# Kernel tuning notes

Hardware: AMD Instinct MI355X
Metric: run time of the kernel (lower is better)

The kernel has to match this reference:

```python
import jax, jax.numpy as jnp
import numpy as np

N = 100000   # nodes
H = 128      # hidden_size
T = 32       # transitivity_size
MD = 16      # mask_dim
K = 3        # propagation steps
E_S = 600000 # spatial edges
E_D = 600000 # dom edges


def setup_inputs() -> dict:
    key = jax.random.key(0)
    ks = jax.random.split(key, 12)
    return {
        "x": jax.random.normal(ks[0], (N, H), jnp.float32),
        "mask": jax.random.uniform(ks[1], (N, MD), jnp.float32),
        "spatial_edge_index": jax.random.randint(ks[2], (2, E_S), 0, N, jnp.int64 if jax.config.jax_enable_x64 else jnp.int32),
        "dom_edge_index": jax.random.randint(ks[3], (2, E_D), 0, N, jnp.int64 if jax.config.jax_enable_x64 else jnp.int32),
        "spatial_edge_attr": jax.random.normal(ks[4], (E_S, 4), jnp.float32),
        "dom_edge_attr": jax.random.normal(ks[5], (E_D, 1), jnp.float32),
        "W_trans": jax.random.normal(ks[6], (2 * H, T), jnp.float32) / np.sqrt(2 * H),
        "b_trans": jnp.zeros((T,), jnp.float32),
        "W_pos": jax.random.normal(ks[7], (4 + T, 1), jnp.float32) / np.sqrt(4 + T),
        "b_pos": jnp.zeros((1,), jnp.float32),
        "W_dom": jax.random.normal(ks[8], (1 + T, 1), jnp.float32) / np.sqrt(1 + T),
        "b_dom": jnp.zeros((1,), jnp.float32),
    }


def _edge_attrs(x, edge_index, W, b):
    # EdgeAttrs: gather src/dst node features, concat, linear + tanh -> [E, T]
    h = jnp.concatenate([x[edge_index[0]], x[edge_index[1]]], axis=1)
    return jnp.tanh(h @ W + b)


def _edge_mask(edge_attr, mask, edge_index, W, b, k_steps, n_nodes):
    # EdgeMask: per-edge gating weight in (0,1), then K rounds of
    # gate-weighted max-propagation of the node mask along edges.
    ew = jax.nn.sigmoid(edge_attr @ W + b)  # [E, 1]
    src, dst = edge_index[0], edge_index[1]
    m = mask
    for _ in range(k_steps):
        msg = m[src] * ew                                  # [E, MD]
        agg = jax.ops.segment_max(msg, dst, num_segments=n_nodes)
        m = jnp.maximum(m, agg)                            # -inf (empty segs) absorbed
    return m, ew


def reference(x, mask, spatial_edge_index, dom_edge_index, spatial_edge_attr,
              dom_edge_attr, W_trans, b_trans, W_pos, b_pos, W_dom, b_dom):
    n_nodes = x.shape[0]
    # spatial branch (projection is dom -> no safe_bc_edges broadcast)
    trans_s = _edge_attrs(x, spatial_edge_index, W_trans, b_trans)
    pos_in = jnp.concatenate([spatial_edge_attr, trans_s], axis=1)  # [E_S, 4+T]
    pos_mask, _pos_ew = _edge_mask(pos_in, mask, spatial_edge_index, W_pos, b_pos, K, n_nodes)
    # dom branch
    trans_d = _edge_attrs(x, dom_edge_index, W_trans, b_trans)
    dom_in = jnp.concatenate([dom_edge_attr, trans_d], axis=1)      # [E_D, 1+T]
    dom_mask, _dom_ew = _edge_mask(dom_in, mask, dom_edge_index, W_dom, b_dom, K, n_nodes)
    return jnp.maximum(mask, jnp.maximum(pos_mask, dom_mask))
```

## Files before the change

kernel.cpp:

```cpp
#include <hip/hip_runtime.h>
#include <hip/hip_bf16.h>
#include <stdint.h>

#define NNODES 100000
#define HID 128
#define TSZ 32
#define MDIM 16
#define ES 600000
#define ED 600000
#define ETOT (ES + ED)
#define GN (2 * NNODES)
#define GNP 200704
#define SCAN_BLOCKS 196
#define N16 (NNODES * MDIM)
#define NP8 (NNODES * 8)
#define GN8 (GN * 8)
#define PQ_BLOCKS 1563
#define N4 (NNODES * 4)

typedef unsigned short ushort_t;

__device__ __forceinline__ float bflo(unsigned u) { return __uint_as_float(u << 16); }
__device__ __forceinline__ float bfhi(unsigned u) { return __uint_as_float(u & 0xffff0000u); }

__device__ __forceinline__ unsigned f2bf(float f) {
    unsigned u = __float_as_uint(f);
    return (u + 0x7FFFu + ((u >> 16) & 1u)) >> 16;
}
__device__ __forceinline__ unsigned packbf(float lo, float hi) {
    return f2bf(lo) | (f2bf(hi) << 16);
}

__device__ __forceinline__ float tanh_fast(float v) {
    float z = __expf(2.f * v);
    return 1.f - 2.f / (z + 1.f);
}

__global__ void k_init(const float* __restrict__ mask, unsigned* __restrict__ m_a,
                       int* __restrict__ counts) {
    int idx = blockIdx.x * 256 + threadIdx.x;
    if (idx < NP8) {
        float2 v = ((const float2*)mask)[idx];
        unsigned p = packbf(v.x, v.y);
        m_a[idx] = p;
        m_a[NP8 + idx] = p;
    }
    if (idx < GNP / 4) ((int4*)counts)[idx] = make_int4(0, 0, 0, 0);
}

__global__ __launch_bounds__(256) void k_pq(const float* __restrict__ x,
                                            const float* __restrict__ Wt,
                                            const float* __restrict__ bt,
                                            char* __restrict__ pq) {
    __shared__ float xs[64][132];
    __shared__ float wl[64][130];
    const int tid = threadIdx.x;
    const int n0 = blockIdx.x * 64;

    for (int i = tid; i < 4096; i += 256) {
        int h = i >> 5, c = i & 31;
        float a = Wt[i];
        float b = Wt[4096 + i];
        wl[c][h] = a;
        wl[c + 32][h] = b;
    }
    const float4* xsrc = (const float4*)(x + (size_t)n0 * 128);
#pragma unroll
    for (int i = 0; i < 8; ++i) {
        int idx = tid + 256 * i;
        int node = idx >> 5;
        int rem = idx & 31;
        if (n0 + node < NNODES) {
            float4 v = xsrc[idx];
            *(float4*)&xs[node][rem * 4] = v;
        }
    }
    __syncthreads();

    const int l = tid & 63;
    const int w = tid >> 6;
    const int c0 = l & 15;
    const int ng = w * 16 + (l >> 4) * 4;
    float acc[4][4] = {};
#pragma unroll 4
    for (int h = 0; h < 128; h += 2) {
        float2 xv[4], wv[4];
#pragma unroll
        for (int m = 0; m < 4; ++m) xv[m] = *(const float2*)&xs[ng + m][h];
#pragma unroll
        for (int m = 0; m < 4; ++m) wv[m] = *(const float2*)&wl[c0 + 16 * m][h];
#pragma unroll
        for (int a = 0; a < 4; ++a)
#pragma unroll
            for (int b = 0; b < 4; ++b)
                acc[a][b] = fmaf(xv[a].y, wv[b].y, fmaf(xv[a].x, wv[b].x, acc[a][b]));
    }
    float bv[4];
#pragma unroll
    for (int b = 0; b < 4; ++b) {
        int c = c0 + 16 * b;
        bv[b] = (c < 32) ? bt[c] : 0.f;
    }
    __syncthreads();
    char* buf = (char*)&xs[0][0];
#pragma unroll
    for (int a = 0; a < 4; ++a) {
#pragma unroll
        for (int b = 0; b < 4; ++b) {
            float v = acc[a][b] + bv[b];
            int q = __float2int_rn(v * 32.f);
            q = max(-127, min(127, q));
            buf[(ng + a) * 64 + c0 + 16 * b] = (char)q;
        }
    }
    __syncthreads();
    uint4 v4 = ((const uint4*)buf)[tid];
    ((uint4*)(pq + (size_t)blockIdx.x * 4096))[tid] = v4;
}

__global__ void k_count(const int* __restrict__ sdst, const int* __restrict__ ddst,
                        int* __restrict__ counts) {
    int e = blockIdx.x * 256 + threadIdx.x;
    if (e >= ETOT) return;
    int gd = (e < ES) ? sdst[e] : (ddst[e - ES] + NNODES);
    atomicAdd(&counts[gd], 1);
}

__global__ __launch_bounds__(256) void k_scan1(const int* __restrict__ counts,
                                               int* __restrict__ bsum) {
    __shared__ int sh[256];
    int tid = threadIdx.x;
    int4 v = ((const int4*)counts)[blockIdx.x * 256 + tid];
    sh[tid] = v.x + v.y + v.z + v.w;
    __syncthreads();
    for (int o = 128; o > 0; o >>= 1) {
        if (tid < o) sh[tid] += sh[tid + o];
        __syncthreads();
    }
    if (tid == 0) bsum[blockIdx.x] = sh[0];
}

__global__ __launch_bounds__(256) void k_scan2(const int* __restrict__ bsum,
                                               int* __restrict__ prefix) {
    __shared__ int sh[256];
    int tid = threadIdx.x;
    int v = (tid < SCAN_BLOCKS) ? bsum[tid] : 0;
    sh[tid] = v;
    __syncthreads();
    for (int o = 1; o < 256; o <<= 1) {
        int add = (tid >= o) ? sh[tid - o] : 0;
        __syncthreads();
        sh[tid] += add;
        __syncthreads();
    }
    prefix[tid] = sh[tid] - v;
}

__global__ __launch_bounds__(256) void k_scan3(const int* __restrict__ counts,
                                               const int* __restrict__ prefix,
                                               int* __restrict__ off,
                                               int* __restrict__ cursor) {
    __shared__ int sh[256];
    int tid = threadIdx.x;
    int4 v = ((const int4*)counts)[blockIdx.x * 256 + tid];
    int tot = v.x + v.y + v.z + v.w;
    sh[tid] = tot;
    __syncthreads();
    for (int o = 1; o < 256; o <<= 1) {
        int add = (tid >= o) ? sh[tid - o] : 0;
        __syncthreads();
        sh[tid] += add;
        __syncthreads();
    }
    int excl = sh[tid] - tot + prefix[blockIdx.x];
    int4 o4;
    o4.x = excl;
    o4.y = o4.x + v.x;
    o4.z = o4.y + v.y;
    o4.w = o4.z + v.z;
    ((int4*)off)[blockIdx.x * 256 + tid] = o4;
    ((int4*)cursor)[blockIdx.x * 256 + tid] = o4;
}

__global__ void k_ewfill(const char* __restrict__ pq,
                         const int* __restrict__ ssrc, const int* __restrict__ sdst,
                         const int* __restrict__ dsrc, const int* __restrict__ ddst,
                         const float* __restrict__ sattr, const float* __restrict__ dattr,
                         const float* __restrict__ Wp, const float* __restrict__ bp,
                         const float* __restrict__ Wd, const float* __restrict__ bd,
                         int* __restrict__ cursor, unsigned* __restrict__ csr) {
    int e = blockIdx.x * 256 + threadIdx.x;
    if (e >= ETOT) return;
    int src, dst, dstg, srcg;
    float acc;
    const float* wt;
    if (e < ES) {
        src = ssrc[e];
        dst = sdst[e];
        dstg = dst;
        srcg = src;
        const float4 a = *(const float4*)(sattr + (size_t)e * 4);
        acc = bp[0] + a.x * Wp[0] + a.y * Wp[1] + a.z * Wp[2] + a.w * Wp[3];
        wt = Wp + 4;
    } else {
        int ed = e - ES;
        src = dsrc[ed];
        dst = ddst[ed];
        dstg = dst + NNODES;
        srcg = src + NNODES;
        acc = bd[0] + dattr[ed] * Wd[0];
        wt = Wd + 1;
    }
    const uint4* Pp = (const uint4*)(pq + (size_t)src * 64);
    const uint4* Qp = (const uint4*)(pq + (size_t)dst * 64 + 32);
    uint4 pa = Pp[0], pb = Pp[1];
    uint4 qa = Qp[0], qb = Qp[1];
    unsigned pw[8] = {pa.x, pa.y, pa.z, pa.w, pb.x, pb.y, pb.z, pb.w};
    unsigned qw[8] = {qa.x, qa.y, qa.z, qa.w, qb.x, qb.y, qb.z, qb.w};
#pragma unroll
    for (int d = 0; d < 8; ++d) {
        unsigned a = pw[d], b = qw[d];
#pragma unroll
        for (int k = 0; k < 4; ++k) {
            int pi = (int)(char)(a >> (8 * k));
            int qi = (int)(char)(b >> (8 * k));
            float t = tanh_fast((float)(pi + qi) * 0.03125f);
            acc = fmaf(t, wt[d * 4 + k], acc);
        }
    }
    float ew = 1.f / (1.f + __expf(-acc));
    unsigned entry = ((unsigned)srcg << 14) | (unsigned)(ew * 16383.f + 0.5f);
    int pos = atomicAdd(&cursor[dstg], 1);
    csr[pos] = entry;
}

template <int BASE, int TAG>
__global__ __launch_bounds__(256) void k_round_t(const unsigned* __restrict__ m_in,
                                                 unsigned* __restrict__ m_out,
                                                 const int* __restrict__ off,
                                                 const unsigned* __restrict__ csr) {
    int idx = blockIdx.x * 256 + threadIdx.x;
    if (idx >= N4) return;
    int g = BASE + (idx >> 2);
    int jp = idx & 3;
    int mi = g * 8 + jp;
    int p0 = off[g], p1 = off[g + 1];
    unsigned c0 = m_in[mi], c1 = m_in[mi + 4];
    float a0 = bflo(c0), b0 = bfhi(c0);
    float a1 = bflo(c1), b1 = bfhi(c1);
    int p = p0;
    for (; p + 1 < p1; p += 2) {
        unsigned e0 = csr[p], e1 = csr[p + 1];
        unsigned s0 = (e0 >> 14) * 8 + jp, s1 = (e1 >> 14) * 8 + jp;
        unsigned m00 = m_in[s0], m01 = m_in[s0 + 4];
        unsigned m10 = m_in[s1], m11 = m_in[s1 + 4];
        float w0 = (float)(e0 & 16383u) * (1.f / 16383.f);
        float w1 = (float)(e1 & 16383u) * (1.f / 16383.f);
        a0 = fmaxf(a0, fmaxf(bflo(m00) * w0, bflo(m10) * w1));
        b0 = fmaxf(b0, fmaxf(bfhi(m00) * w0, bfhi(m10) * w1));
        a1 = fmaxf(a1, fmaxf(bflo(m01) * w0, bflo(m11) * w1));
        b1 = fmaxf(b1, fmaxf(bfhi(m01) * w0, bfhi(m11) * w1));
    }
    if (p < p1) {
        unsigned e0 = csr[p];
        unsigned s0 = (e0 >> 14) * 8 + jp;
        unsigned m00 = m_in[s0], m01 = m_in[s0 + 4];
        float w0 = (float)(e0 & 16383u) * (1.f / 16383.f);
        a0 = fmaxf(a0, bflo(m00) * w0);
        b0 = fmaxf(b0, bfhi(m00) * w0);
        a1 = fmaxf(a1, bflo(m01) * w0);
        b1 = fmaxf(b1, bfhi(m01) * w0);
    }
    m_out[mi] = packbf(a0, b0);
    m_out[mi + 4] = packbf(a1, b1);
}

__global__ __launch_bounds__(256) void k_round_final(const unsigned* __restrict__ m_in,
                                                     float* __restrict__ out,
                                                     const int* __restrict__ off,
                                                     const unsigned* __restrict__ csr) {
    int idx = blockIdx.x * 256 + threadIdx.x;
    if (idx >= N4) return;
    int g = idx >> 2;
    int jp = idx & 3;
    float a0, b0, a1, b1;
    {
        int mi = g * 8 + jp;
        unsigned c0 = m_in[mi], c1 = m_in[mi + 4];
        a0 = bflo(c0); b0 = bfhi(c0);
        a1 = bflo(c1); b1 = bfhi(c1);
    }
    {
        int p0 = off[g], p1 = off[g + 1];
        for (int p = p0; p < p1; ++p) {
            unsigned e0 = csr[p];
            unsigned s0 = (e0 >> 14) * 8 + jp;
            unsigned m00 = m_in[s0], m01 = m_in[s0 + 4];
            float w0 = (float)(e0 & 16383u) * (1.f / 16383.f);
            a0 = fmaxf(a0, bflo(m00) * w0);
            b0 = fmaxf(b0, bfhi(m00) * w0);
            a1 = fmaxf(a1, bflo(m01) * w0);
            b1 = fmaxf(b1, bfhi(m01) * w0);
        }
    }
    {
        int mi2 = (g + NNODES) * 8 + jp;
        unsigned c0 = m_in[mi2], c1 = m_in[mi2 + 4];
        a0 = fmaxf(a0, bflo(c0)); b0 = fmaxf(b0, bfhi(c0));
        a1 = fmaxf(a1, bflo(c1)); b1 = fmaxf(b1, bfhi(c1));
        int g2 = g + NNODES;
        int p0 = off[g2], p1 = off[g2 + 1];
        for (int p = p0; p < p1; ++p) {
            unsigned e0 = csr[p];
            unsigned s0 = (e0 >> 14) * 8 + jp;
            unsigned m00 = m_in[s0], m01 = m_in[s0 + 4];
            float w0 = (float)(e0 & 16383u) * (1.f / 16383.f);
            a0 = fmaxf(a0, bflo(m00) * w0);
            b0 = fmaxf(b0, bfhi(m00) * w0);
            a1 = fmaxf(a1, bflo(m01) * w0);
            b1 = fmaxf(b1, bfhi(m01) * w0);
        }
    }
    *(float2*)&out[g * 16 + jp * 2] = make_float2(a0, b0);
    *(float2*)&out[g * 16 + jp * 2 + 8] = make_float2(a1, b1);
}

extern "C" void kernel_launch(void* const* d_in, const int* in_sizes, int n_in,
                              void* d_out, int out_size, void* d_ws, size_t ws_size,
                              hipStream_t stream) {
    const float* x     = (const float*)d_in[0];
    const float* mask  = (const float*)d_in[1];
    const int*   sei   = (const int*)d_in[2];
    const int*   dei   = (const int*)d_in[3];
    const float* sattr = (const float*)d_in[4];
    const float* dattr = (const float*)d_in[5];
    const float* Wt    = (const float*)d_in[6];
    const float* bt    = (const float*)d_in[7];
    const float* Wp    = (const float*)d_in[8];
    const float* bp    = (const float*)d_in[9];
    const float* Wd    = (const float*)d_in[10];
    const float* bd    = (const float*)d_in[11];
    float* out = (float*)d_out;

    char* ws = (char*)d_ws;
    size_t o = 0;
    auto take = [&](size_t bytes) -> char* {
        char* p = ws + o;
        o = (o + bytes + 255) & ~(size_t)255;
        return p;
    };
    char* pq     = take((size_t)PQ_BLOCKS * 4096);
    int* counts  = (int*)take((size_t)GNP * 4);
    int* off     = (int*)take((size_t)GNP * 4);
    int* cursor  = (int*)take((size_t)GNP * 4);
    int* bsum    = (int*)take(256 * 4);
    int* prefix  = (int*)take(256 * 4);
    unsigned* csr = (unsigned*)take((size_t)ETOT * 4);
    unsigned* m_a = (unsigned*)take((size_t)GN8 * 4);
    unsigned* m_b = (unsigned*)take((size_t)GN8 * 4);

    const int RB = (N4 + 255) / 256;

    k_init<<<3125, 256, 0, stream>>>(mask, m_a, counts);
    k_pq<<<PQ_BLOCKS, 256, 0, stream>>>(x, Wt, bt, pq);
    k_count<<<(ETOT + 255) / 256, 256, 0, stream>>>(sei + ES, dei + ED, counts);
    k_scan1<<<SCAN_BLOCKS, 256, 0, stream>>>(counts, bsum);
    k_scan2<<<1, 256, 0, stream>>>(bsum, prefix);
    k_scan3<<<SCAN_BLOCKS, 256, 0, stream>>>(counts, prefix, off, cursor);
    k_ewfill<<<(ETOT + 255) / 256, 256, 0, stream>>>(pq,
        sei, sei + ES, dei, dei + ED, sattr, dattr, Wp, bp, Wd, bd, cursor, csr);
    k_round_t<0, 0><<<RB, 256, 0, stream>>>(m_a, m_b, off, csr);
    k_round_t<NNODES, 1><<<RB, 256, 0, stream>>>(m_a, m_b, off, csr);
    k_round_t<0, 2><<<RB, 256, 0, stream>>>(m_b, m_a, off, csr);
    k_round_t<NNODES, 3><<<RB, 256, 0, stream>>>(m_b, m_a, off, csr);
    k_round_final<<<RB, 256, 0, stream>>>(m_a, out, off, csr);
}
```

Before: 332.5 us.

## Fuse init/count and scan kernels, merge per-branch propagation rounds into single launches

Merges mask packing and edge in-degree counting into one kernel with int4-vectorised destination loads, and zeroes counts with a memset. Replaces the three-kernel scan with one kernel that waits on a global atomic flag spin barrier across its 196 blocks. Also runs both graph branches in a single launch per propagation round, cutting the number of kernel launches. The grid barrier assumes all scan blocks are resident at the same time, which is a deadlock risk if they are not.

```diff
diff --git a/kernel.cpp b/kernel.cpp
--- a/kernel.cpp
+++ b/kernel.cpp
@@ -12,11 +12,11 @@
 #define GN (2 * NNODES)
 #define GNP 200704
 #define SCAN_BLOCKS 196
-#define N16 (NNODES * MDIM)
 #define NP8 (NNODES * 8)
 #define GN8 (GN * 8)
 #define PQ_BLOCKS 1563
 #define N4 (NNODES * 4)
+#define CNT_BLK 586
 
 typedef unsigned short ushort_t;
 
@@ -34,18 +34,6 @@
 __device__ __forceinline__ float tanh_fast(float v) {
     float z = __expf(2.f * v);
     return 1.f - 2.f / (z + 1.f);
-}
-
-__global__ void k_init(const float* __restrict__ mask, unsigned* __restrict__ m_a,
-                       int* __restrict__ counts) {
-    int idx = blockIdx.x * 256 + threadIdx.x;
-    if (idx < NP8) {
-        float2 v = ((const float2*)mask)[idx];
-        unsigned p = packbf(v.x, v.y);
-        m_a[idx] = p;
-        m_a[NP8 + idx] = p;
-    }
-    if (idx < GNP / 4) ((int4*)counts)[idx] = make_int4(0, 0, 0, 0);
 }
 
 __global__ __launch_bounds__(256) void k_pq(const float* __restrict__ x,
@@ -118,34 +106,49 @@
     ((uint4*)(pq + (size_t)blockIdx.x * 4096))[tid] = v4;
 }
 
-__global__ void k_count(const int* __restrict__ sdst, const int* __restrict__ ddst,
-                        int* __restrict__ counts) {
-    int e = blockIdx.x * 256 + threadIdx.x;
-    if (e >= ETOT) return;
-    int gd = (e < ES) ? sdst[e] : (ddst[e - ES] + NNODES);
-    atomicAdd(&counts[gd], 1);
-}
-
-__global__ __launch_bounds__(256) void k_scan1(const int* __restrict__ counts,
-                                               int* __restrict__ bsum) {
+__global__ __launch_bounds__(256) void k_initcount(const float* __restrict__ mask,
+                                                   unsigned* __restrict__ m_a,
+                                                   const int* __restrict__ sdst,
+                                                   const int* __restrict__ ddst,
+                                                   int* __restrict__ counts) {
+    const int tid = threadIdx.x;
+    int b = (int)blockIdx.x;
+    if (b < 3125) {
+        int idx = b * 256 + tid;
+        float2 v = ((const float2*)mask)[idx];
+        unsigned p = packbf(v.x, v.y);
+        m_a[idx] = p;
+        m_a[NP8 + idx] = p;
+        return;
+    }
+    b -= 3125;
+    const int* dst;
+    int add;
+    if (b < CNT_BLK) { dst = sdst; add = 0; }
+    else { b -= CNT_BLK; dst = ddst; add = NNODES; }
+    int e0 = (b * 256 + tid) * 4;
+    if (e0 + 4 <= 600000) {
+        int4 d = *(const int4*)(dst + e0);
+        atomicAdd(&counts[d.x + add], 1);
+        atomicAdd(&counts[d.y + add], 1);
+        atomicAdd(&counts[d.z + add], 1);
+        atomicAdd(&counts[d.w + add], 1);
+    } else {
+        for (int e = e0; e < 600000; ++e) atomicAdd(&counts[dst[e] + add], 1);
+    }
+}
+
+__global__ __launch_bounds__(256) void k_scanfused(const int* __restrict__ counts,
+                                                   int* __restrict__ bsum,
+                                                   int* __restrict__ flag,
+                                                   int* __restrict__ off,
+                                                   int* __restrict__ cursor) {
     __shared__ int sh[256];
-    int tid = threadIdx.x;
-    int4 v = ((const int4*)counts)[blockIdx.x * 256 + tid];
-    sh[tid] = v.x + v.y + v.z + v.w;
-    __syncthreads();
-    for (int o = 128; o > 0; o >>= 1) {
-        if (tid < o) sh[tid] += sh[tid + o];
-        __syncthreads();
-    }
-    if (tid == 0) bsum[blockIdx.x] = sh[0];
-}
-
-__global__ __launch_bounds__(256) void k_scan2(const int* __restrict__ bsum,
-                                               int* __restrict__ prefix) {
-    __shared__ int sh[256];
-    int tid = threadIdx.x;
-    int v = (tid < SCAN_BLOCKS) ? bsum[tid] : 0;
-    sh[tid] = v;
+    const int tid = threadIdx.x;
+    const int bid = (int)blockIdx.x;
+    int4 v = ((const int4*)counts)[bid * 256 + tid];
+    int tot = v.x + v.y + v.z + v.w;
+    sh[tid] = tot;
     __syncthreads();
     for (int o = 1; o < 256; o <<= 1) {
         int add = (tid >= o) ? sh[tid - o] : 0;
@@ -153,18 +156,16 @@
         sh[tid] += add;
         __syncthreads();
     }
-    prefix[tid] = sh[tid] - v;
-}
-
-__global__ __launch_bounds__(256) void k_scan3(const int* __restrict__ counts,
-                                               const int* __restrict__ prefix,
-                                               int* __restrict__ off,
-                                               int* __restrict__ cursor) {
-    __shared__ int sh[256];
-    int tid = threadIdx.x;
-    int4 v = ((const int4*)counts)[blockIdx.x * 256 + tid];
-    int tot = v.x + v.y + v.z + v.w;
-    sh[tid] = tot;
+    int incl = sh[tid];
+    if (tid == 255) bsum[bid] = incl;
+    if (tid == 0) {
+        __threadfence();
+        atomicAdd(flag, 1);
+        while (__hip_atomic_load(flag, __ATOMIC_RELAXED, __HIP_MEMORY_SCOPE_AGENT) < SCAN_BLOCKS) {}
+        __threadfence();
+    }
+    __syncthreads();
+    sh[tid] = (tid < SCAN_BLOCKS) ? bsum[tid] : 0;
     __syncthreads();
     for (int o = 1; o < 256; o <<= 1) {
         int add = (tid >= o) ? sh[tid - o] : 0;
@@ -172,14 +173,15 @@
         sh[tid] += add;
         __syncthreads();
     }
-    int excl = sh[tid] - tot + prefix[blockIdx.x];
+    int base = (bid > 0) ? sh[bid - 1] : 0;
+    int excl = base + incl - tot;
     int4 o4;
     o4.x = excl;
     o4.y = o4.x + v.x;
     o4.z = o4.y + v.y;
     o4.w = o4.z + v.z;
-    ((int4*)off)[blockIdx.x * 256 + tid] = o4;
-    ((int4*)cursor)[blockIdx.x * 256 + tid] = o4;
+    ((int4*)off)[bid * 256 + tid] = o4;
+    ((int4*)cursor)[bid * 256 + tid] = o4;
 }
 
 __global__ void k_ewfill(const char* __restrict__ pq,
@@ -234,14 +236,13 @@
     csr[pos] = entry;
 }
 
-template <int BASE, int TAG>
+template <int TAG>
 __global__ __launch_bounds__(256) void k_round_t(const unsigned* __restrict__ m_in,
                                                  unsigned* __restrict__ m_out,
                                                  const int* __restrict__ off,
                                                  const unsigned* __restrict__ csr) {
     int idx = blockIdx.x * 256 + threadIdx.x;
-    if (idx >= N4) return;
-    int g = BASE + (idx >> 2);
+    int g = idx >> 2;
     int jp = idx & 3;
     int mi = g * 8 + jp;
     int p0 = off[g], p1 = off[g + 1];
@@ -349,29 +350,23 @@
         o = (o + bytes + 255) & ~(size_t)255;
         return p;
     };
-    char* pq     = take((size_t)PQ_BLOCKS * 4096);
-    int* counts  = (int*)take((size_t)GNP * 4);
-    int* off     = (int*)take((size_t)GNP * 4);
-    int* cursor  = (int*)take((size_t)GNP * 4);
-    int* bsum    = (int*)take(256 * 4);
-    int* prefix  = (int*)take(256 * 4);
+    char* pq      = take((size_t)PQ_BLOCKS * 4096);
+    int* counts   = (int*)take((size_t)GNP * 4 + 256);
+    int* flag     = counts + GNP;
+    int* off      = (int*)take((size_t)GNP * 4);
+    int* cursor   = (int*)take((size_t)GNP * 4);
+    int* bsum     = (int*)take(256 * 4);
     unsigned* csr = (unsigned*)take((size_t)ETOT * 4);
     unsigned* m_a = (unsigned*)take((size_t)GN8 * 4);
     unsigned* m_b = (unsigned*)take((size_t)GN8 * 4);
 
-    const int RB = (N4 + 255) / 256;
-
-    k_init<<<3125, 256, 0, stream>>>(mask, m_a, counts);
+    hipMemsetAsync(counts, 0, (size_t)GNP * 4 + 256, stream);
     k_pq<<<PQ_BLOCKS, 256, 0, stream>>>(x, Wt, bt, pq);
-    k_count<<<(ETOT + 255) / 256, 256, 0, stream>>>(sei + ES, dei + ED, counts);
-    k_scan1<<<SCAN_BLOCKS, 256, 0, stream>>>(counts, bsum);
-    k_scan2<<<1, 256, 0, stream>>>(bsum, prefix);
-    k_scan3<<<SCAN_BLOCKS, 256, 0, stream>>>(counts, prefix, off, cursor);
+    k_initcount<<<3125 + 2 * CNT_BLK, 256, 0, stream>>>(mask, m_a, sei + ES, dei + ED, counts);
+    k_scanfused<<<SCAN_BLOCKS, 256, 0, stream>>>(counts, bsum, flag, off, cursor);
     k_ewfill<<<(ETOT + 255) / 256, 256, 0, stream>>>(pq,
         sei, sei + ES, dei, dei + ED, sattr, dattr, Wp, bp, Wd, bd, cursor, csr);
-    k_round_t<0, 0><<<RB, 256, 0, stream>>>(m_a, m_b, off, csr);
-    k_round_t<NNODES, 1><<<RB, 256, 0, stream>>>(m_a, m_b, off, csr);
-    k_round_t<0, 2><<<RB, 256, 0, stream>>>(m_b, m_a, off, csr);
-    k_round_t<NNODES, 3><<<RB, 256, 0, stream>>>(m_b, m_a, off, csr);
-    k_round_final<<<RB, 256, 0, stream>>>(m_a, out, off, csr);
-}
+    k_round_t<0><<<3125, 256, 0, stream>>>(m_a, m_b, off, csr);
+    k_round_t<1><<<3125, 256, 0, stream>>>(m_b, m_a, off, csr);
+    k_round_final<<<1563, 256, 0, stream>>>(m_a, out, off, csr);
+}
```

Result: slower. 341.7 us (+2.8%).
